# Kernel optimization log

Measured on AMD Instinct MI355X. Metric: run time of the kernel, lower is better.

Reference implementation:

```python
import jax, jax.numpy as jnp
import numpy as np

DIM = 384; HEADS = 6; K = 10; G = 2
GC = DIM // G            # group channel dim
HD = DIM // HEADS        # head dim
SCALE = HD ** -0.5
LN_EPS = 1e-5


def _sqdist(a, b):
    # a: [..., n, 3], b: [..., m, 3] -> [..., n, m]
    return (jnp.sum(a * a, -1)[..., :, None]
            + jnp.sum(b * b, -1)[..., None, :]
            - 2.0 * jnp.einsum('...nc,...mc->...nm', a, b))


def setup_inputs() -> dict:
    key = jax.random.key(0)
    ks = jax.random.split(key, 12)
    B, N, M = 4, 1024, 1024
    s = 0.02
    return {
        'q': jax.random.normal(ks[0], (B, N, DIM), jnp.float32),
        'q_pos': jax.random.normal(ks[1], (B, N, 3), jnp.float32),
        'v': jax.random.normal(ks[2], (B, M, DIM), jnp.float32),
        'v_pos': jax.random.normal(ks[3], (B, M, 3), jnp.float32),
        'Wq': jax.random.normal(ks[4], (DIM, DIM), jnp.float32) * s,
        'Wk': jax.random.normal(ks[5], (DIM, DIM), jnp.float32) * s,
        'Wv': jax.random.normal(ks[6], (DIM, DIM), jnp.float32) * s,
        'Wvoff': jax.random.normal(ks[7], (DIM, DIM), jnp.float32) * s,
        'Woff1': jax.random.normal(ks[8], (DIM, 2 * GC), jnp.float32) * s,
        'boff1': jnp.zeros((DIM,), jnp.float32),
        'ln_g': jnp.ones((DIM,), jnp.float32),
        'ln_b': jnp.zeros((DIM,), jnp.float32),
        'Woff2': jax.random.normal(ks[9], (3, DIM), jnp.float32) * s,
        'Wproj': jax.random.normal(ks[10], (DIM, DIM), jnp.float32) * s,
        'bproj': jnp.zeros((DIM,), jnp.float32),
    }


def reference(q, q_pos, v, v_pos, Wq, Wk, Wv, Wvoff, Woff1, boff1,
              ln_g, ln_b, Woff2, Wproj, bproj):
    B, N, C = q.shape
    M = v.shape[1]

    # --- knn_point: K nearest v_pos for each q_pos ---
    idx = jax.lax.top_k(-_sqdist(q_pos, v_pos), K)[1]        # [B,N,K]
    idx_flat = idx.reshape(B, N * K, 1)

    qp = q @ Wq.T                                            # [B,N,C]
    v_off = v @ Wvoff.T                                      # [B,M,C]

    # index_points gathers
    local_v = jnp.take_along_axis(v_off, idx_flat, axis=1).reshape(B, N, K, C)
    local_v_pos = jnp.take_along_axis(v_pos, idx_flat, axis=1).reshape(B, N, K, 3)

    # group split: 'b n k (g c) -> b g n k c'
    off_local_v = local_v.reshape(B, N, K, G, GC).transpose(0, 3, 1, 2, 4)  # [B,G,N,K,GC]
    group_q = qp.reshape(B, N, G, GC).transpose(0, 2, 1, 3)                 # [B,G,N,GC]

    shift_feat = jnp.concatenate(
        [off_local_v, jnp.broadcast_to(group_q[:, :, :, None, :], (B, G, N, K, GC))], -1)

    # linear_offset MLP: Linear -> LayerNorm -> GELU(exact) -> Linear, then tanh
    h = shift_feat @ Woff1.T + boff1                          # [B,G,N,K,DIM]
    mu = h.mean(-1, keepdims=True)
    var = h.var(-1, keepdims=True)
    h = (h - mu) / jnp.sqrt(var + LN_EPS) * ln_g + ln_b
    h = jax.nn.gelu(h, approximate=False)
    offset = jnp.tanh(h @ Woff2.T)                            # [B,G,N,K,3]

    shift_pos = (local_v_pos[:, None] + offset).reshape(B, G, N * K, 3)
    vg = v.reshape(B, M, G, GC).transpose(0, 2, 1, 3)         # [B,G,M,GC]

    # --- three_nn + reciprocal-distance three_interpolate ---
    sqd = _sqdist(shift_pos, v_pos[:, None])                  # [B,G,N*K,M]
    negd, idx3 = jax.lax.top_k(-sqd, 3)                       # 3 smallest
    dist = jnp.sqrt(jnp.maximum(-negd, 0.0))                  # [B,G,N*K,3]
    w = 1.0 / (dist + 1e-8)
    w = w / jnp.sum(w, -1, keepdims=True)
    feats = jnp.take_along_axis(vg, idx3.reshape(B, G, N * K * 3, 1), axis=2)
    feats = feats.reshape(B, G, N * K, 3, GC)
    interp = jnp.einsum('bgnj,bgnjc->bgnc', w, feats)         # [B,G,N*K,GC]
    # '(b g) (n k) c -> b n k (g c)'
    interp = interp.reshape(B, G, N, K, GC).transpose(0, 2, 3, 1, 4).reshape(B, N, K, C)

    # --- local cross-attention (each query attends to its K interpolated feats) ---
    kf = (interp @ Wk.T).reshape(B, N, K, HEADS, HD)
    vf = (interp @ Wv.T).reshape(B, N, K, HEADS, HD)
    qh = qp.reshape(B, N, HEADS, HD)
    attn = jnp.einsum('bnhd,bnkhd->bhnk', qh, kf) * SCALE
    attn = jax.nn.softmax(attn, axis=-1)
    out = jnp.einsum('bhnk,bnkhd->bnhd', attn, vf).reshape(B, N, C)
    return out @ Wproj.T + bproj
```

## Files before the change

### kernel.cpp

```cpp
#include <hip/hip_runtime.h>
#include <math.h>

#define NB 4
#define NN 1024
#define NM 1024
#define NC 384
#define NK 10
#define NG 2
#define NGC 192
#define NH 6

#define GSZ ((size_t)NB * NM * NC)

#define OFF_WQ 0
#define OFF_W1B 147456
#define OFF_WK0 221184
#define OFF_WK1 294912
#define OFF_WV0 368640
#define OFF_WV1 442368
#define OFF_WPROJ 516096
#define WT_ALL_FLOATS 663552

__device__ __forceinline__ float wred_sum(float v) {
#pragma unroll
  for (int m = 32; m >= 1; m >>= 1) v += __shfl_xor(v, m, 64);
  return v;
}

__device__ __forceinline__ void wred_argmin(float& d, int& m) {
#pragma unroll
  for (int off = 32; off >= 1; off >>= 1) {
    float od = __shfl_xor(d, off, 64);
    int om = __shfl_xor(m, off, 64);
    if (od < d || (od == d && om < m)) { d = od; m = om; }
  }
}

__global__ void transpose_all_k(const float* __restrict__ Wq, const float* __restrict__ Woff1,
                                const float* __restrict__ Wk, const float* __restrict__ Wv,
                                const float* __restrict__ Wproj, float* __restrict__ Wt_all) {
  const float* W;
  int i0, icount, doff;
  switch (blockIdx.y) {
    case 0: W = Wq;    i0 = 0;   icount = NC;  doff = OFF_WQ;    break;
    case 1: W = Woff1; i0 = NGC; icount = NGC; doff = OFF_W1B;   break;
    case 2: W = Wk;    i0 = 0;   icount = NGC; doff = OFF_WK0;   break;
    case 3: W = Wk;    i0 = NGC; icount = NGC; doff = OFF_WK1;   break;
    case 4: W = Wv;    i0 = 0;   icount = NGC; doff = OFF_WV0;   break;
    case 5: W = Wv;    i0 = NGC; icount = NGC; doff = OFF_WV1;   break;
    default: W = Wproj; i0 = 0;  icount = NC;  doff = OFF_WPROJ; break;
  }
  int id = blockIdx.x * 256 + threadIdx.x;
  if (id >= icount * NC) return;
  int o = id % NC;
  int i = id / NC;
  Wt_all[doff + (size_t)i * NC + o] = W[(size_t)o * NC + i0 + i];
}

__global__ void wcomb_k(const float* __restrict__ Woff1, const float* __restrict__ Wvoff,
                        float* __restrict__ Wcomb_t) {
  int o = blockIdx.x;
  int g = blockIdx.y;
  int i = threadIdx.x;
  __shared__ float w1[NGC];
  if (i < NGC) w1[i] = Woff1[(size_t)o * NC + i];
  __syncthreads();
  float acc = 0.f;
#pragma unroll 4
  for (int j = 0; j < NGC; ++j)
    acc = fmaf(w1[j], Wvoff[(size_t)(g * NGC + j) * NC + i], acc);
  Wcomb_t[((size_t)g * NC + i) * NC + o] = acc;
}

__global__ __launch_bounds__(384) void linear2_k(const float* __restrict__ X, int IN,
                                                 const float* __restrict__ Wt,
                                                 const float* __restrict__ bias,
                                                 float* __restrict__ Y) {
  __shared__ __align__(16) float xs[NC][20];
  int tid = threadIdx.x;
  int og = tid % 96, rg = tid / 96;
  int r0 = blockIdx.x * 16;
  for (int t = tid; t < 16 * IN; t += 384) {
    int r = t / IN, kk = t % IN;
    xs[kk][r] = X[(size_t)(r0 + r) * NC + kk];
  }
  __syncthreads();
  float acc[4][4];
#pragma unroll
  for (int i = 0; i < 4; ++i)
#pragma unroll
    for (int j = 0; j < 4; ++j) acc[i][j] = 0.f;
  int o = og * 4;
#pragma unroll 4
  for (int kk = 0; kk < IN; ++kk) {
    float4 w4 = *(const float4*)&Wt[(size_t)kk * NC + o];
    float4 x4 = *(const float4*)&xs[kk][rg * 4];
    float xr[4] = {x4.x, x4.y, x4.z, x4.w};
    float wr[4] = {w4.x, w4.y, w4.z, w4.w};
#pragma unroll
    for (int ri = 0; ri < 4; ++ri)
#pragma unroll
      for (int oi = 0; oi < 4; ++oi) acc[ri][oi] = fmaf(xr[ri], wr[oi], acc[ri][oi]);
  }
  float4 bv = make_float4(0.f, 0.f, 0.f, 0.f);
  if (bias) bv = *(const float4*)&bias[o];
#pragma unroll
  for (int ri = 0; ri < 4; ++ri) {
    float4 ov;
    ov.x = acc[ri][0] + bv.x;
    ov.y = acc[ri][1] + bv.y;
    ov.z = acc[ri][2] + bv.z;
    ov.w = acc[ri][3] + bv.w;
    *(float4*)&Y[(size_t)(r0 + rg * 4 + ri) * NC + o] = ov;
  }
}

__global__ __launch_bounds__(384) void vproj_k(const float* __restrict__ v,
                                               const float* __restrict__ Wcomb_t,
                                               const float* __restrict__ Wt_all,
                                               float* __restrict__ vcontrib,
                                               float* __restrict__ KcT,
                                               float* __restrict__ VcT) {
  __shared__ __align__(16) float xs[NC][20];
  int tid = threadIdx.x;
  int og = tid % 96, rg = tid / 96;
  int r0 = blockIdx.x * 16;
  for (int t = tid; t < 16 * NC; t += 384) {
    int r = t / NC, kk = t % NC;
    xs[kk][r] = v[(size_t)(r0 + r) * NC + kk];
  }
  __syncthreads();
  const float* Wj[6] = {Wcomb_t,           Wcomb_t + (size_t)NC * NC,
                        Wt_all + OFF_WK0,  Wt_all + OFF_WK1,
                        Wt_all + OFF_WV0,  Wt_all + OFF_WV1};
  float* Yj[6] = {vcontrib, vcontrib + GSZ, KcT, KcT + GSZ, VcT, VcT + GSZ};
  const int inj[6] = {NC, NC, NGC, NGC, NGC, NGC};
  const int xoj[6] = {0, 0, 0, NGC, 0, NGC};
  int o = og * 4;
#pragma unroll
  for (int job = 0; job < 6; ++job) {
    const float* Wt = Wj[job];
    float* Y = Yj[job];
    const int IN = inj[job], xoff = xoj[job];
    float acc[4][4];
#pragma unroll
    for (int i = 0; i < 4; ++i)
#pragma unroll
      for (int j = 0; j < 4; ++j) acc[i][j] = 0.f;
#pragma unroll 4
    for (int kk = 0; kk < IN; ++kk) {
      float4 w4 = *(const float4*)&Wt[(size_t)kk * NC + o];
      float4 x4 = *(const float4*)&xs[xoff + kk][rg * 4];
      float xr[4] = {x4.x, x4.y, x4.z, x4.w};
      float wr[4] = {w4.x, w4.y, w4.z, w4.w};
#pragma unroll
      for (int ri = 0; ri < 4; ++ri)
#pragma unroll
        for (int oi = 0; oi < 4; ++oi) acc[ri][oi] = fmaf(xr[ri], wr[oi], acc[ri][oi]);
    }
#pragma unroll
    for (int ri = 0; ri < 4; ++ri)
      *(float4*)&Y[(size_t)(r0 + rg * 4 + ri) * NC + o] =
          make_float4(acc[ri][0], acc[ri][1], acc[ri][2], acc[ri][3]);
  }
}

__global__ __launch_bounds__(384) void qproj_k(const float* __restrict__ q,
                                               const float* __restrict__ Wt_all,
                                               float* __restrict__ qp,
                                               float* __restrict__ qcontrib) {
  __shared__ __align__(16) float xs[NC][20];
  int tid = threadIdx.x;
  int og = tid % 96, rg = tid / 96;
  int r0 = blockIdx.x * 16;
  for (int t = tid; t < 16 * NC; t += 384) {
    int r = t / NC, kk = t % NC;
    xs[kk][r] = q[(size_t)(r0 + r) * NC + kk];
  }
  __syncthreads();
  int o = og * 4;
  const float* Wqt = Wt_all + OFF_WQ;
  float acc[4][4];
#pragma unroll
  for (int i = 0; i < 4; ++i)
#pragma unroll
    for (int j = 0; j < 4; ++j) acc[i][j] = 0.f;
#pragma unroll 4
  for (int kk = 0; kk < NC; ++kk) {
    float4 w4 = *(const float4*)&Wqt[(size_t)kk * NC + o];
    float4 x4 = *(const float4*)&xs[kk][rg * 4];
    float xr[4] = {x4.x, x4.y, x4.z, x4.w};
    float wr[4] = {w4.x, w4.y, w4.z, w4.w};
#pragma unroll
    for (int ri = 0; ri < 4; ++ri)
#pragma unroll
      for (int oi = 0; oi < 4; ++oi) acc[ri][oi] = fmaf(xr[ri], wr[oi], acc[ri][oi]);
  }
#pragma unroll
  for (int ri = 0; ri < 4; ++ri)
    *(float4*)&qp[(size_t)(r0 + rg * 4 + ri) * NC + o] =
        make_float4(acc[ri][0], acc[ri][1], acc[ri][2], acc[ri][3]);
  __syncthreads();
#pragma unroll
  for (int ri = 0; ri < 4; ++ri)
#pragma unroll
    for (int oi = 0; oi < 4; ++oi) xs[o + oi][rg * 4 + ri] = acc[ri][oi];
  __syncthreads();
  const float* W1b = Wt_all + OFF_W1B;
#pragma unroll
  for (int g = 0; g < NG; ++g) {
    float a2[4][4];
#pragma unroll
    for (int i = 0; i < 4; ++i)
#pragma unroll
      for (int j = 0; j < 4; ++j) a2[i][j] = 0.f;
#pragma unroll 4
    for (int kk = 0; kk < NGC; ++kk) {
      float4 w4 = *(const float4*)&W1b[(size_t)kk * NC + o];
      float4 x4 = *(const float4*)&xs[g * NGC + kk][rg * 4];
      float xr[4] = {x4.x, x4.y, x4.z, x4.w};
      float wr[4] = {w4.x, w4.y, w4.z, w4.w};
#pragma unroll
      for (int ri = 0; ri < 4; ++ri)
#pragma unroll
        for (int oi = 0; oi < 4; ++oi) a2[ri][oi] = fmaf(xr[ri], wr[oi], a2[ri][oi]);
    }
    float* Yg = qcontrib + (size_t)g * NB * NN * NC;
#pragma unroll
    for (int ri = 0; ri < 4; ++ri)
      *(float4*)&Yg[(size_t)(r0 + rg * 4 + ri) * NC + o] =
          make_float4(a2[ri][0], a2[ri][1], a2[ri][2], a2[ri][3]);
  }
}

__global__ __launch_bounds__(256) void knn2_k(const float* __restrict__ q_pos,
                                              const float* __restrict__ v_pos,
                                              int* __restrict__ knn_idx) {
  __shared__ float px[NM], py[NM], pz[NM], ss[NM];
  int tid = threadIdx.x, lane = tid & 63, wid = tid >> 6;
  int b = blockIdx.x / (NN / 4);
  int n = (blockIdx.x % (NN / 4)) * 4 + wid;
  for (int t = tid; t < NM; t += 256) {
    float x = v_pos[((size_t)b * NM + t) * 3 + 0];
    float y = v_pos[((size_t)b * NM + t) * 3 + 1];
    float z = v_pos[((size_t)b * NM + t) * 3 + 2];
    px[t] = x; py[t] = y; pz[t] = z;
    ss[t] = x * x + y * y + z * z;
  }
  __syncthreads();
  float qx = q_pos[((size_t)b * NN + n) * 3 + 0];
  float qy = q_pos[((size_t)b * NN + n) * 3 + 1];
  float qz = q_pos[((size_t)b * NN + n) * 3 + 2];
  float qq = qx * qx + qy * qy + qz * qz;
  float bd[NK];
  int bi[NK];
#pragma unroll
  for (int j = 0; j < NK; ++j) { bd[j] = 1e30f; bi[j] = 0x7fffffff; }
#pragma unroll
  for (int t = 0; t < NM / 64; ++t) {
    int m = t * 64 + lane;
    float d = qq + ss[m] - 2.f * (qx * px[m] + qy * py[m] + qz * pz[m]);
    if (d < bd[NK - 1]) {
#pragma unroll
      for (int j = NK - 1; j > 0; --j) {
        if (d < bd[j - 1]) { bd[j] = bd[j - 1]; bi[j] = bi[j - 1]; }
        else if (d < bd[j]) { bd[j] = d; bi[j] = m; }
      }
      if (d < bd[0]) { bd[0] = d; bi[0] = m; }
    }
  }
  size_t base = ((size_t)b * NN + n) * NK;
#pragma unroll
  for (int round = 0; round < NK; ++round) {
    float dh = bd[0];
    int mh = bi[0];
    wred_argmin(dh, mh);
    if (lane == 0) knn_idx[base + round] = mh;
    if (bi[0] == mh) {
#pragma unroll
      for (int j = 0; j < NK - 1; ++j) { bd[j] = bd[j + 1]; bi[j] = bi[j + 1]; }
      bd[NK - 1] = 1e30f; bi[NK - 1] = 0x7fffffff;
    }
  }
}

__global__ __launch_bounds__(256) void mlp3nn_k(
    const float* __restrict__ vcontrib, const float* __restrict__ qcontrib,
    const float* __restrict__ boff1, const float* __restrict__ ln_g,
    const float* __restrict__ ln_b, const float* __restrict__ Woff2,
    const int* __restrict__ knn_idx, const float* __restrict__ v_pos,
    int* __restrict__ idx3, float* __restrict__ w3) {
  __shared__ float px[NM], py[NM], pz[NM], ss[NM];
  int tid = threadIdx.x, lane = tid & 63, wid = tid >> 6;
  int r = blockIdx.x * 4 + wid;
  int b = (blockIdx.x * 4) / (NK * NN * NG);
  for (int t = tid; t < NM; t += 256) {
    float x = v_pos[((size_t)b * NM + t) * 3 + 0];
    float y = v_pos[((size_t)b * NM + t) * 3 + 1];
    float z = v_pos[((size_t)b * NM + t) * 3 + 2];
    px[t] = x; py[t] = y; pz[t] = z;
    ss[t] = x * x + y * y + z * z;
  }
  __syncthreads();
  int k = r % NK;
  int n = (r / NK) % NN;
  int g = (r / (NK * NN)) % NG;
  int m = knn_idx[((size_t)b * NN + n) * NK + k];
  const float* vc = vcontrib + ((size_t)(g * NB + b) * NM + m) * NC;
  const float* qc = qcontrib + ((size_t)(g * NB + b) * NN + n) * NC;
  float h[6];
  float s = 0.f, s2 = 0.f;
#pragma unroll
  for (int j = 0; j < 6; ++j) {
    int c = j * 64 + lane;
    float x = vc[c] + qc[c] + boff1[c];
    h[j] = x; s += x; s2 += x * x;
  }
  s = wred_sum(s);
  s2 = wred_sum(s2);
  float mean = s * (1.f / NC);
  float var = s2 * (1.f / NC) - mean * mean;
  float inv = 1.f / sqrtf(var + 1e-5f);
  float p0 = 0.f, p1 = 0.f, p2 = 0.f;
#pragma unroll
  for (int j = 0; j < 6; ++j) {
    int c = j * 64 + lane;
    float x = (h[j] - mean) * inv * ln_g[c] + ln_b[c];
    x = 0.5f * x * (1.f + erff(x * 0.70710678118654752f));
    p0 = fmaf(x, Woff2[0 * NC + c], p0);
    p1 = fmaf(x, Woff2[1 * NC + c], p1);
    p2 = fmaf(x, Woff2[2 * NC + c], p2);
  }
  p0 = wred_sum(p0);
  p1 = wred_sum(p1);
  p2 = wred_sum(p2);
  float sx = px[m] + tanhf(p0);
  float sy = py[m] + tanhf(p1);
  float sz = pz[m] + tanhf(p2);
  float qq2 = sx * sx + sy * sy + sz * sz;
  float d0v = 1e30f, d1v = 1e30f, d2v = 1e30f;
  int i0v = 0x7fffffff, i1v = 0x7fffffff, i2v = 0x7fffffff;
#pragma unroll
  for (int t = 0; t < NM / 64; ++t) {
    int m2 = t * 64 + lane;
    float d = qq2 + ss[m2] - 2.f * (sx * px[m2] + sy * py[m2] + sz * pz[m2]);
    if (d < d2v) {
      d2v = d; i2v = m2;
      if (d2v < d1v) { float td = d1v; d1v = d2v; d2v = td; int ti = i1v; i1v = i2v; i2v = ti; }
      if (d1v < d0v) { float td = d0v; d0v = d1v; d1v = td; int ti = i0v; i0v = i1v; i1v = ti; }
    }
  }
  float rd[3];
  int rm[3];
#pragma unroll
  for (int round = 0; round < 3; ++round) {
    float dh = d0v;
    int mh = i0v;
    wred_argmin(dh, mh);
    rd[round] = dh; rm[round] = mh;
    if (i0v == mh) {
      d0v = d1v; i0v = i1v;
      d1v = d2v; i1v = i2v;
      d2v = 1e30f; i2v = 0x7fffffff;
    }
  }
  if (lane == 0) {
    float e0 = 1.f / (sqrtf(fmaxf(rd[0], 0.f)) + 1e-8f);
    float e1 = 1.f / (sqrtf(fmaxf(rd[1], 0.f)) + 1e-8f);
    float e2 = 1.f / (sqrtf(fmaxf(rd[2], 0.f)) + 1e-8f);
    float sw = e0 + e1 + e2;
    idx3[(size_t)r * 3 + 0] = rm[0]; w3[(size_t)r * 3 + 0] = e0 / sw;
    idx3[(size_t)r * 3 + 1] = rm[1]; w3[(size_t)r * 3 + 1] = e1 / sw;
    idx3[(size_t)r * 3 + 2] = rm[2]; w3[(size_t)r * 3 + 2] = e2 / sw;
  }
}

__global__ __launch_bounds__(NC) void attn_k(const float* __restrict__ qp,
                                             const float* __restrict__ Kc,
                                             const float* __restrict__ Vc,
                                             const int* __restrict__ idx3,
                                             const float* __restrict__ w3,
                                             float* __restrict__ attn_out) {
  __shared__ float vfs[NK][NC];
  __shared__ float lgs[NH][NK];
  __shared__ int il[NG][NK][3];
  __shared__ float wl[NG][NK][3];
  int o = threadIdx.x;
  int lane = o & 63, wid = o >> 6;
  int b = blockIdx.x / NN;
  int n = blockIdx.x % NN;
  if (o < NG * NK * 3) {
    int g = o / (NK * 3), k = (o / 3) % NK, j = o % 3;
    size_t rr = (((size_t)(b * NG + g) * NN + n) * NK + k) * 3 + j;
    il[g][k][j] = idx3[rr];
    wl[g][k][j] = w3[rr];
  }
  __syncthreads();
  float qv = qp[((size_t)b * NN + n) * NC + o];
  for (int k = 0; k < NK; ++k) {
    float kf = 0.f, vf = 0.f;
#pragma unroll
    for (int g = 0; g < NG; ++g)
#pragma unroll
      for (int j = 0; j < 3; ++j) {
        int m = il[g][k][j];
        float w = wl[g][k][j];
        size_t base = ((size_t)(g * NB + b) * NM + m) * NC + o;
        kf = fmaf(w, Kc[base], kf);
        vf = fmaf(w, Vc[base], vf);
      }
    vfs[k][o] = vf;
    float p = wred_sum(qv * kf);
    if (lane == 0) lgs[wid][k] = p * 0.125f;
  }
  __syncthreads();
  float a[NK];
  float mx = -1e30f;
#pragma unroll
  for (int k = 0; k < NK; ++k) { a[k] = lgs[wid][k]; mx = fmaxf(mx, a[k]); }
  float sum = 0.f;
#pragma unroll
  for (int k = 0; k < NK; ++k) { a[k] = expf(a[k] - mx); sum += a[k]; }
  float outv = 0.f;
#pragma unroll
  for (int k = 0; k < NK; ++k) outv = fmaf(a[k] / sum, vfs[k][o], outv);
  attn_out[((size_t)b * NN + n) * NC + o] = outv;
}

extern "C" void kernel_launch(void* const* d_in, const int* in_sizes, int n_in,
                              void* d_out, int out_size, void* d_ws, size_t ws_size,
                              hipStream_t stream) {
  (void)in_sizes; (void)n_in; (void)out_size; (void)ws_size;
  const float* q     = (const float*)d_in[0];
  const float* q_pos = (const float*)d_in[1];
  const float* v     = (const float*)d_in[2];
  const float* v_pos = (const float*)d_in[3];
  const float* Wq    = (const float*)d_in[4];
  const float* Wk    = (const float*)d_in[5];
  const float* Wv    = (const float*)d_in[6];
  const float* Wvoff = (const float*)d_in[7];
  const float* Woff1 = (const float*)d_in[8];
  const float* boff1 = (const float*)d_in[9];
  const float* ln_g  = (const float*)d_in[10];
  const float* ln_b  = (const float*)d_in[11];
  const float* Woff2 = (const float*)d_in[12];
  const float* Wproj = (const float*)d_in[13];
  const float* bproj = (const float*)d_in[14];
  float* out = (float*)d_out;

  char* p = (char*)d_ws;
  auto alloc_f = [&](size_t n) { float* r = (float*)p; p += n * sizeof(float); return r; };
  auto alloc_i = [&](size_t n) { int* r = (int*)p; p += n * sizeof(int); return r; };

  float* qp        = alloc_f((size_t)NB * NN * NC);
  float* qcontrib  = alloc_f((size_t)NG * NB * NN * NC);
  float* vcontrib  = alloc_f((size_t)NG * NB * NM * NC);
  float* KcT       = alloc_f((size_t)NG * NB * NM * NC);
  float* VcT       = alloc_f((size_t)NG * NB * NM * NC);
  float* Wt_all    = alloc_f((size_t)WT_ALL_FLOATS);
  float* Wcomb_t   = alloc_f((size_t)NG * NC * NC);
  float* w3        = alloc_f((size_t)NB * NG * NN * NK * 3);
  int* knn_idx     = alloc_i((size_t)NB * NN * NK);
  int* idx3        = alloc_i((size_t)NB * NG * NN * NK * 3);
  float* attn_out  = vcontrib;

  transpose_all_k<<<dim3(576, 7), 256, 0, stream>>>(Wq, Woff1, Wk, Wv, Wproj, Wt_all);
  wcomb_k<<<dim3(NC, NG), NC, 0, stream>>>(Woff1, Wvoff, Wcomb_t);

  qproj_k<<<NB * NN / 16, 384, 0, stream>>>(q, Wt_all, qp, qcontrib);
  knn2_k<<<NB * (NN / 4), 256, 0, stream>>>(q_pos, v_pos, knn_idx);
  vproj_k<<<NB * NM / 16, 384, 0, stream>>>(v, Wcomb_t, Wt_all, vcontrib, KcT, VcT);

  mlp3nn_k<<<NB * NG * NN * NK / 4, 256, 0, stream>>>(vcontrib, qcontrib, boff1, ln_g, ln_b,
                                                      Woff2, knn_idx, v_pos, idx3, w3);
  attn_k<<<NB * NN, NC, 0, stream>>>(qp, KcT, VcT, idx3, w3, attn_out);
  linear2_k<<<NB * NN / 16, 384, 0, stream>>>(attn_out, NC, Wt_all + OFF_WPROJ, bproj, out);
}
```

Baseline: 543.3 us.

## Split fused projection kernels into per-job grid dimension for more parallelism

The six sequential projection jobs in vproj_k are spread across blockIdx.y, so each block runs one job and the grid grows six-fold. qproj_k is split into a generic gemm16_k launch for Wq and a second launch with a job dimension for the two group qcontrib projections, and linear2_k is folded into the same generic kernel. The aim is to give the GPU more blocks to fill its compute units. In exchange, v and qp are reloaded into shared memory once per job and there is one extra launch.

```diff
diff --git a/kernel.cpp b/kernel.cpp
--- a/kernel.cpp
+++ b/kernel.cpp
@@ -72,17 +72,21 @@
   Wcomb_t[((size_t)g * NC + i) * NC + o] = acc;
 }
 
-__global__ __launch_bounds__(384) void linear2_k(const float* __restrict__ X, int IN,
-                                                 const float* __restrict__ Wt,
-                                                 const float* __restrict__ bias,
-                                                 float* __restrict__ Y) {
+__global__ __launch_bounds__(384) void gemm16_k(const float* __restrict__ X, int IN, int xoff0,
+                                                int xoff_stride, const float* __restrict__ Wt0,
+                                                size_t wstride, const float* __restrict__ bias,
+                                                float* __restrict__ Y0, size_t ystride) {
   __shared__ __align__(16) float xs[NC][20];
   int tid = threadIdx.x;
   int og = tid % 96, rg = tid / 96;
   int r0 = blockIdx.x * 16;
+  int job = blockIdx.y;
+  int xoff = xoff0 + job * xoff_stride;
+  const float* Wt = Wt0 + (size_t)job * wstride;
+  float* Y = Y0 + (size_t)job * ystride;
   for (int t = tid; t < 16 * IN; t += 384) {
     int r = t / IN, kk = t % IN;
-    xs[kk][r] = X[(size_t)(r0 + r) * NC + kk];
+    xs[kk][r] = X[(size_t)(r0 + r) * NC + xoff + kk];
   }
   __syncthreads();
   float acc[4][4];
@@ -125,69 +129,32 @@
   int tid = threadIdx.x;
   int og = tid % 96, rg = tid / 96;
   int r0 = blockIdx.x * 16;
-  for (int t = tid; t < 16 * NC; t += 384) {
-    int r = t / NC, kk = t % NC;
-    xs[kk][r] = v[(size_t)(r0 + r) * NC + kk];
-  }
-  __syncthreads();
-  const float* Wj[6] = {Wcomb_t,           Wcomb_t + (size_t)NC * NC,
-                        Wt_all + OFF_WK0,  Wt_all + OFF_WK1,
-                        Wt_all + OFF_WV0,  Wt_all + OFF_WV1};
-  float* Yj[6] = {vcontrib, vcontrib + GSZ, KcT, KcT + GSZ, VcT, VcT + GSZ};
-  const int inj[6] = {NC, NC, NGC, NGC, NGC, NGC};
-  const int xoj[6] = {0, 0, 0, NGC, 0, NGC};
+  int job = blockIdx.y;
+  const float* Wt;
+  float* Y;
+  int IN, xoff;
+  switch (job) {
+    case 0: Wt = Wcomb_t;                 Y = vcontrib;       IN = NC;  xoff = 0;   break;
+    case 1: Wt = Wcomb_t + (size_t)NC * NC; Y = vcontrib + GSZ; IN = NC;  xoff = 0;   break;
+    case 2: Wt = Wt_all + OFF_WK0;        Y = KcT;            IN = NGC; xoff = 0;   break;
+    case 3: Wt = Wt_all + OFF_WK1;        Y = KcT + GSZ;      IN = NGC; xoff = NGC; break;
+    case 4: Wt = Wt_all + OFF_WV0;        Y = VcT;            IN = NGC; xoff = 0;   break;
+    default: Wt = Wt_all + OFF_WV1;       Y = VcT + GSZ;      IN = NGC; xoff = NGC; break;
+  }
+  for (int t = tid; t < 16 * IN; t += 384) {
+    int r = t / IN, kk = t % IN;
+    xs[kk][r] = v[(size_t)(r0 + r) * NC + xoff + kk];
+  }
+  __syncthreads();
+  float acc[4][4];
+#pragma unroll
+  for (int i = 0; i < 4; ++i)
+#pragma unroll
+    for (int j = 0; j < 4; ++j) acc[i][j] = 0.f;
   int o = og * 4;
-#pragma unroll
-  for (int job = 0; job < 6; ++job) {
-    const float* Wt = Wj[job];
-    float* Y = Yj[job];
-    const int IN = inj[job], xoff = xoj[job];
-    float acc[4][4];
-#pragma unroll
-    for (int i = 0; i < 4; ++i)
-#pragma unroll
-      for (int j = 0; j < 4; ++j) acc[i][j] = 0.f;
 #pragma unroll 4
-    for (int kk = 0; kk < IN; ++kk) {
-      float4 w4 = *(const float4*)&Wt[(size_t)kk * NC + o];
-      float4 x4 = *(const float4*)&xs[xoff + kk][rg * 4];
-      float xr[4] = {x4.x, x4.y, x4.z, x4.w};
-      float wr[4] = {w4.x, w4.y, w4.z, w4.w};
-#pragma unroll
-      for (int ri = 0; ri < 4; ++ri)
-#pragma unroll
-        for (int oi = 0; oi < 4; ++oi) acc[ri][oi] = fmaf(xr[ri], wr[oi], acc[ri][oi]);
-    }
-#pragma unroll
-    for (int ri = 0; ri < 4; ++ri)
-      *(float4*)&Y[(size_t)(r0 + rg * 4 + ri) * NC + o] =
-          make_float4(acc[ri][0], acc[ri][1], acc[ri][2], acc[ri][3]);
-  }
-}
-
-__global__ __launch_bounds__(384) void qproj_k(const float* __restrict__ q,
-                                               const float* __restrict__ Wt_all,
-                                               float* __restrict__ qp,
-                                               float* __restrict__ qcontrib) {
-  __shared__ __align__(16) float xs[NC][20];
-  int tid = threadIdx.x;
-  int og = tid % 96, rg = tid / 96;
-  int r0 = blockIdx.x * 16;
-  for (int t = tid; t < 16 * NC; t += 384) {
-    int r = t / NC, kk = t % NC;
-    xs[kk][r] = q[(size_t)(r0 + r) * NC + kk];
-  }
-  __syncthreads();
-  int o = og * 4;
-  const float* Wqt = Wt_all + OFF_WQ;
-  float acc[4][4];
-#pragma unroll
-  for (int i = 0; i < 4; ++i)
-#pragma unroll
-    for (int j = 0; j < 4; ++j) acc[i][j] = 0.f;
-#pragma unroll 4
-  for (int kk = 0; kk < NC; ++kk) {
-    float4 w4 = *(const float4*)&Wqt[(size_t)kk * NC + o];
+  for (int kk = 0; kk < IN; ++kk) {
+    float4 w4 = *(const float4*)&Wt[(size_t)kk * NC + o];
     float4 x4 = *(const float4*)&xs[kk][rg * 4];
     float xr[4] = {x4.x, x4.y, x4.z, x4.w};
     float wr[4] = {w4.x, w4.y, w4.z, w4.w};
@@ -198,39 +165,8 @@
   }
 #pragma unroll
   for (int ri = 0; ri < 4; ++ri)
-    *(float4*)&qp[(size_t)(r0 + rg * 4 + ri) * NC + o] =
+    *(float4*)&Y[(size_t)(r0 + rg * 4 + ri) * NC + o] =
         make_float4(acc[ri][0], acc[ri][1], acc[ri][2], acc[ri][3]);
-  __syncthreads();
-#pragma unroll
-  for (int ri = 0; ri < 4; ++ri)
-#pragma unroll
-    for (int oi = 0; oi < 4; ++oi) xs[o + oi][rg * 4 + ri] = acc[ri][oi];
-  __syncthreads();
-  const float* W1b = Wt_all + OFF_W1B;
-#pragma unroll
-  for (int g = 0; g < NG; ++g) {
-    float a2[4][4];
-#pragma unroll
-    for (int i = 0; i < 4; ++i)
-#pragma unroll
-      for (int j = 0; j < 4; ++j) a2[i][j] = 0.f;
-#pragma unroll 4
-    for (int kk = 0; kk < NGC; ++kk) {
-      float4 w4 = *(const float4*)&W1b[(size_t)kk * NC + o];
-      float4 x4 = *(const float4*)&xs[g * NGC + kk][rg * 4];
-      float xr[4] = {x4.x, x4.y, x4.z, x4.w};
-      float wr[4] = {w4.x, w4.y, w4.z, w4.w};
-#pragma unroll
-      for (int ri = 0; ri < 4; ++ri)
-#pragma unroll
-        for (int oi = 0; oi < 4; ++oi) a2[ri][oi] = fmaf(xr[ri], wr[oi], a2[ri][oi]);
-    }
-    float* Yg = qcontrib + (size_t)g * NB * NN * NC;
-#pragma unroll
-    for (int ri = 0; ri < 4; ++ri)
-      *(float4*)&Yg[(size_t)(r0 + rg * 4 + ri) * NC + o] =
-          make_float4(a2[ri][0], a2[ri][1], a2[ri][2], a2[ri][3]);
-  }
 }
 
 __global__ __launch_bounds__(256) void knn2_k(const float* __restrict__ q_pos,
@@ -467,12 +403,16 @@
   transpose_all_k<<<dim3(576, 7), 256, 0, stream>>>(Wq, Woff1, Wk, Wv, Wproj, Wt_all);
   wcomb_k<<<dim3(NC, NG), NC, 0, stream>>>(Woff1, Wvoff, Wcomb_t);
 
-  qproj_k<<<NB * NN / 16, 384, 0, stream>>>(q, Wt_all, qp, qcontrib);
+  gemm16_k<<<dim3(NB * NN / 16, 1), 384, 0, stream>>>(q, NC, 0, 0, Wt_all + OFF_WQ, 0, nullptr,
+                                                      qp, 0);
   knn2_k<<<NB * (NN / 4), 256, 0, stream>>>(q_pos, v_pos, knn_idx);
-  vproj_k<<<NB * NM / 16, 384, 0, stream>>>(v, Wcomb_t, Wt_all, vcontrib, KcT, VcT);
+  gemm16_k<<<dim3(NB * NN / 16, 2), 384, 0, stream>>>(qp, NGC, 0, NGC, Wt_all + OFF_W1B, 0,
+                                                      nullptr, qcontrib, (size_t)NB * NN * NC);
+  vproj_k<<<dim3(NB * NM / 16, 6), 384, 0, stream>>>(v, Wcomb_t, Wt_all, vcontrib, KcT, VcT);
 
   mlp3nn_k<<<NB * NG * NN * NK / 4, 256, 0, stream>>>(vcontrib, qcontrib, boff1, ln_g, ln_b,
                                                       Woff2, knn_idx, v_pos, idx3, w3);
   attn_k<<<NB * NN, NC, 0, stream>>>(qp, KcT, VcT, idx3, w3, attn_out);
-  linear2_k<<<NB * NN / 16, 384, 0, stream>>>(attn_out, NC, Wt_all + OFF_WPROJ, bproj, out);
-}
+  gemm16_k<<<dim3(NB * NN / 16, 1), 384, 0, stream>>>(attn_out, NC, 0, 0, Wt_all + OFF_WPROJ, 0,
+                                                      bproj, out, 0);
+}
```

Result: faster. 475.0 us (-12.6%).
